# Kernel optimization log

Hardware: AMD Instinct MI355X
Metric: run time of the kernel (lower is better)

## Reference

```python
import jax, jax.numpy as jnp
import numpy as np

N_NODES = 50000
N_EDGES = 500000
N_GRAPHS = 16
C_IN = 2
CO_T = 64
CO_S = 16
K = 3


def conv_glu(x, w, b):
    # x: (N, Cin, T), w: (2*Cout, Cin, K), b: (2*Cout,) -> (N, Cout, T-K+1)
    y = jax.lax.conv_general_dilated(x, w, (1,), 'VALID',
                                     dimension_numbers=('NCH', 'OIH', 'NCH'))
    y = y + b[None, :, None]
    a, g = jnp.split(y, 2, axis=1)
    return a * jax.nn.sigmoid(g)


def gcn_relu(x, W, b, row, col, n_nodes):
    # GCNConv with self-loops, unit edge weights, applied to all T slices at once.
    # x: (N, Cin, T), W: (Cin, Cout), b: (Cout,)
    xw = jnp.einsum('nct,cd->ndt', x, W)  # (N, Cout, T)
    deg = jnp.zeros((n_nodes,), x.dtype).at[col].add(1.0) + 1.0  # +1 self loop
    dinv = deg ** -0.5
    coef = (dinv[row] * dinv[col])[:, None, None]
    msg = xw[row] * coef                   # (E, Cout, T) gather
    agg = jax.ops.segment_sum(msg, col, num_segments=n_nodes)
    agg = agg + xw * (dinv ** 2)[:, None, None]  # self-loop term
    return jax.nn.relu(agg + b[None, :, None])


def gap(x, batch, n_graphs):
    # global mean pool over nodes per graph; x: (N, C, T) -> (B, C, T)
    s = jax.ops.segment_sum(x, batch, num_segments=n_graphs)
    cnt = jax.ops.segment_sum(jnp.ones((x.shape[0],), x.dtype), batch, num_segments=n_graphs)
    return s / jnp.maximum(cnt, 1.0)[:, None, None]


def setup_inputs() -> dict:
    key = jax.random.key(0)
    ks = jax.random.split(key, 16)
    x = jax.random.normal(ks[0], (N_NODES, C_IN, 12), dtype=jnp.float32)
    edge_index = jax.random.randint(ks[1], (2, N_EDGES), 0, N_NODES)
    batch = jnp.sort(jax.random.randint(ks[2], (N_NODES,), 0, N_GRAPHS))

    def conv_p(k, cin, cout):
        k1, k2 = jax.random.split(k)
        fan = cin * K
        bound = 1.0 / np.sqrt(fan)
        w = jax.random.uniform(k1, (2 * cout, cin, K), jnp.float32, -bound, bound)
        b = jax.random.uniform(k2, (2 * cout,), jnp.float32, -bound, bound)
        return w, b

    w_t1a, b_t1a = conv_p(ks[3], C_IN, CO_T)
    w_t1b, b_t1b = conv_p(ks[4], CO_S, CO_T)
    w_t2a, b_t2a = conv_p(ks[5], CO_T, CO_T)
    w_t2b, b_t2b = conv_p(ks[6], CO_S, CO_T)

    def gcn_p(k, cin, cout):
        k1, k2 = jax.random.split(k)
        w = jax.random.normal(k1, (cin, cout), jnp.float32) * (1.0 / np.sqrt(cin))
        b = jnp.zeros((cout,), jnp.float32)
        return w, b

    w_s1, bb_s1 = gcn_p(ks[7], CO_T, CO_S)
    w_s2, bb_s2 = gcn_p(ks[8], CO_T, CO_S)

    return dict(x=x, edge_index=edge_index, batch=batch,
                w_t1a=w_t1a, b_t1a=b_t1a, w_s1=w_s1, bb_s1=bb_s1,
                w_t1b=w_t1b, b_t1b=b_t1b, w_t2a=w_t2a, b_t2a=b_t2a,
                w_s2=w_s2, bb_s2=bb_s2, w_t2b=w_t2b, b_t2b=b_t2b)


def reference(x, edge_index, batch, w_t1a, b_t1a, w_s1, bb_s1, w_t1b, b_t1b,
              w_t2a, b_t2a, w_s2, bb_s2, w_t2b, b_t2b):
    row, col = edge_index[0], edge_index[1]
    h = conv_glu(x, w_t1a, b_t1a)                     # (N, 64, 10)
    h = gcn_relu(h, w_s1, bb_s1, row, col, N_NODES)   # (N, 16, 10)
    h = conv_glu(h, w_t1b, b_t1b)                     # (N, 64, 8)
    h = conv_glu(h, w_t2a, b_t2a)                     # (N, 64, 6)
    h = gcn_relu(h, w_s2, bb_s2, row, col, N_NODES)   # (N, 16, 6)
    h = gap(h, batch, N_GRAPHS)                       # (B, 16, 6)
    out = conv_glu(h, w_t2b, b_t2b)                   # (B, 64, 4)
    return out
```

## Files before the change

kernel.cpp:

```cpp
#include <hip/hip_runtime.h>
#include <hip/hip_bf16.h>


#define NN 50000
#define NE 500000
#define NG 16
#define CAP 64

typedef __attribute__((ext_vector_type(8))) short bf16x8;
typedef __attribute__((ext_vector_type(8))) unsigned short u16x8;
typedef __attribute__((ext_vector_type(4))) float f32x4;

__device__ __forceinline__ float sigf(float g) {
    return 1.0f / (1.0f + __expf(-g));
}

__device__ __forceinline__ unsigned short to_bf16(float f) {
    __bf16 b = (__bf16)f;
    return __builtin_bit_cast(unsigned short, b);
}

__device__ __forceinline__ float from_bf16(unsigned short u) {
    return __uint_as_float(((unsigned)u) << 16);
}

__global__ void k_fill(const int* __restrict__ row, const int* __restrict__ col,
                       int* __restrict__ cnt, unsigned short* __restrict__ bucket,
                       int E)
{
    int e = blockIdx.x * 256 + threadIdx.x;
    if (e >= E) return;
    int c = col[e];
    int pos = atomicAdd(&cnt[c], 1);
    if (pos < CAP) bucket[(size_t)c * CAP + pos] = (unsigned short)row[e];
}

__global__ void k_prep2(const float* __restrict__ w1b, const float* __restrict__ w2a,
                        const float* __restrict__ ws2,
                        unsigned short* __restrict__ A2h,
                        unsigned short* __restrict__ A3h,
                        unsigned short* __restrict__ APh)
{
    int idx = blockIdx.x * 256 + threadIdx.x;
    if (idx < 1024) {
        int lane = idx & 63; int r = idx >> 6; int s = r & 1; int T = r >> 1;
        int m = T * 16 + (lane & 15); int g = lane >> 4;
        for (int i = 0; i < 8; ++i) {
            int k = s * 32 + 8 * g + i;
            float w = 0.f;
            if (k < 48) { int ci = k & 15, kk = k >> 4; w = w1b[m * 48 + ci * 3 + kk]; }
            A2h[idx * 8 + i] = to_bf16(w);
        }
    }
    if (idx < 3072) {
        int lane = idx & 63; int r = idx >> 6; int s = r % 6; int T = r / 6;
        int m = T * 16 + (lane & 15); int g = lane >> 4;
        for (int i = 0; i < 8; ++i) {
            int k = s * 32 + 8 * g + i;
            int ci = k & 63, kk = k >> 6;
            A3h[idx * 8 + i] = to_bf16(w2a[m * 192 + ci * 3 + kk]);
        }
    }
    if (idx < 128) {
        int lane = idx & 63; int s = idx >> 6;
        int d = lane & 15; int g = lane >> 4;
        for (int i = 0; i < 8; ++i) {
            int co = s * 32 + 8 * g + i;
            APh[idx * 8 + i] = to_bf16(ws2[co * 16 + d]);
        }
    }
}

__global__ __launch_bounds__(256) void k_conv1_proj2(
    const float* __restrict__ x, const float* __restrict__ w,
    const float* __restrict__ b, const float* __restrict__ W1,
    const int* __restrict__ cnt, unsigned short* __restrict__ xwb, int nNodes)
{
    __shared__ float pk[64 * 28];
    __shared__ float bs[128];
    int tid = threadIdx.x;
    for (int i = tid; i < 1792; i += 256) {
        int c = i / 28, q = i - c * 28;
        float v;
        if (q < 6)       v = w[c * 6 + q];
        else if (q < 12) v = w[(c + 64) * 6 + (q - 6)];
        else             v = W1[c * 16 + (q - 12)];
        pk[i] = v;
    }
    if (tid < 128) bs[tid] = b[tid];
    __syncthreads();

    int idx = blockIdx.x * 256 + tid;
    if (idx >= nNodes * 5) return;
    int n = idx / 5, p = idx - n * 5;
    int t0 = 2 * p;

    float xq[2][4];
#pragma unroll
    for (int ci = 0; ci < 2; ++ci) {
        const float* xp = &x[n * 24 + ci * 12 + t0];
        float2 u0 = *(const float2*)(xp);
        float2 u1 = *(const float2*)(xp + 2);
        xq[ci][0] = u0.x; xq[ci][1] = u0.y; xq[ci][2] = u1.x; xq[ci][3] = u1.y;
    }

    float acc0[16], acc1[16];
#pragma unroll
    for (int d = 0; d < 16; ++d) { acc0[d] = 0.f; acc1[d] = 0.f; }

    for (int c = 0; c < 64; ++c) {
        const float* P = &pk[c * 28];
        float4 A = *(const float4*)(P);
        float4 B = *(const float4*)(P + 4);
        float4 C = *(const float4*)(P + 8);
        float bc = bs[c], bg = bs[c + 64];

        float a0 = bc, g0 = bg;
        a0 = fmaf(A.x, xq[0][0], a0); a0 = fmaf(A.y, xq[0][1], a0); a0 = fmaf(A.z, xq[0][2], a0);
        a0 = fmaf(A.w, xq[1][0], a0); a0 = fmaf(B.x, xq[1][1], a0); a0 = fmaf(B.y, xq[1][2], a0);
        g0 = fmaf(B.z, xq[0][0], g0); g0 = fmaf(B.w, xq[0][1], g0); g0 = fmaf(C.x, xq[0][2], g0);
        g0 = fmaf(C.y, xq[1][0], g0); g0 = fmaf(C.z, xq[1][1], g0); g0 = fmaf(C.w, xq[1][2], g0);
        float h0 = a0 * sigf(g0);

        float a1 = bc, g1 = bg;
        a1 = fmaf(A.x, xq[0][1], a1); a1 = fmaf(A.y, xq[0][2], a1); a1 = fmaf(A.z, xq[0][3], a1);
        a1 = fmaf(A.w, xq[1][1], a1); a1 = fmaf(B.x, xq[1][2], a1); a1 = fmaf(B.y, xq[1][3], a1);
        g1 = fmaf(B.z, xq[0][1], g1); g1 = fmaf(B.w, xq[0][2], g1); g1 = fmaf(C.x, xq[0][3], g1);
        g1 = fmaf(C.y, xq[1][1], g1); g1 = fmaf(C.z, xq[1][2], g1); g1 = fmaf(C.w, xq[1][3], g1);
        float h1 = a1 * sigf(g1);

        float4 D = *(const float4*)(P + 12);
        float4 E = *(const float4*)(P + 16);
        float4 F = *(const float4*)(P + 20);
        float4 G = *(const float4*)(P + 24);
        float wr[16] = {D.x, D.y, D.z, D.w, E.x, E.y, E.z, E.w,
                        F.x, F.y, F.z, F.w, G.x, G.y, G.z, G.w};
#pragma unroll
        for (int d = 0; d < 16; ++d) {
            acc0[d] = fmaf(wr[d], h0, acc0[d]);
            acc1[d] = fmaf(wr[d], h1, acc1[d]);
        }
    }
    float dv = rsqrtf((float)cnt[n] + 1.0f);
    u16x8 p0, p1, p2_, p3_;
#pragma unroll
    for (int d = 0; d < 8; ++d) {
        p0[d]  = to_bf16(acc0[d] * dv);
        p1[d]  = to_bf16(acc0[d + 8] * dv);
        p2_[d] = to_bf16(acc1[d] * dv);
        p3_[d] = to_bf16(acc1[d + 8] * dv);
    }
    unsigned short* o = &xwb[n * 160 + t0 * 16];
    *(u16x8*)(o)      = p0;
    *(u16x8*)(o + 8)  = p1;
    *(u16x8*)(o + 16) = p2_;
    *(u16x8*)(o + 24) = p3_;
}

template <int W8>
__global__ __launch_bounds__(256) void k_gather_bf(
    const unsigned short* __restrict__ xs, const unsigned short* __restrict__ bucket,
    const int* __restrict__ cnt, const float* __restrict__ bias,
    unsigned short* __restrict__ hb, int total)
{
    constexpr int W = W8 * 8;
    int idx = blockIdx.x * 256 + threadIdx.x;
    if (idx >= total) return;
    int c = idx / W8, ch = idx - c * W8;
    const int deg = min(cnt[c], CAP);
    const size_t choff = (size_t)ch * 8;

    float acc[8];
#pragma unroll
    for (int i = 0; i < 8; ++i) acc[i] = 0.f;

    for (int j = 0; j < deg; j += 4) {
        ushort4 id4 = *(const ushort4*)&bucket[(size_t)c * CAP + j];
        {
            u16x8 v = *(const u16x8*)&xs[(size_t)id4.x * W + choff];
#pragma unroll
            for (int i = 0; i < 8; ++i) acc[i] += from_bf16(v[i]);
        }
        if (j + 1 < deg) {
            u16x8 v = *(const u16x8*)&xs[(size_t)id4.y * W + choff];
#pragma unroll
            for (int i = 0; i < 8; ++i) acc[i] += from_bf16(v[i]);
        }
        if (j + 2 < deg) {
            u16x8 v = *(const u16x8*)&xs[(size_t)id4.z * W + choff];
#pragma unroll
            for (int i = 0; i < 8; ++i) acc[i] += from_bf16(v[i]);
        }
        if (j + 3 < deg) {
            u16x8 v = *(const u16x8*)&xs[(size_t)id4.w * W + choff];
#pragma unroll
            for (int i = 0; i < 8; ++i) acc[i] += from_bf16(v[i]);
        }
    }

    const float dv = rsqrtf((float)cnt[c] + 1.0f);
    u16x8 sv = *(const u16x8*)&xs[(size_t)c * W + choff];
    const float* bp = &bias[(ch & 1) * 8];
    float4 b0 = *(const float4*)(bp);
    float4 b1 = *(const float4*)(bp + 4);
    float bb[8] = {b0.x, b0.y, b0.z, b0.w, b1.x, b1.y, b1.z, b1.w};
    u16x8 o;
#pragma unroll
    for (int i = 0; i < 8; ++i)
        o[i] = to_bf16(fmaxf(dv * (acc[i] + from_bf16(sv[i])) + bb[i], 0.f));
    *(u16x8*)&hb[(size_t)c * W + choff] = o;
}

__global__ __launch_bounds__(256) void k_conv23_v18(
    const unsigned short* __restrict__ h2b,
    const unsigned short* __restrict__ A2h, const float* __restrict__ b1b,
    const unsigned short* __restrict__ A3h, const float* __restrict__ b2a,
    const unsigned short* __restrict__ APh, const int* __restrict__ cnt,
    unsigned short* __restrict__ xw2b)
{
    __shared__ unsigned short H[11520];

    const int tid  = threadIdx.x;
    const int wid  = tid >> 6;
    const int lane = tid & 63;
    const int base = blockIdx.x * 16;

    unsigned short* H2 = H;
    unsigned short* H3 = H;

    const int nn   = lane & 15;
    const int nb   = nn >> 3;
    const int tt   = nn & 7;
    const int g    = lane >> 4;
    const int rowb = g * 4;

    for (int i = tid; i < 320; i += 256) {
        int ns = i / 20, rem = i - ns * 20;
        int t = rem >> 1, ci0 = (rem & 1) * 8;
        u16x8 v = *(const u16x8*)&h2b[(size_t)(base + ns) * 160 + t * 16 + ci0];
        *(u16x8*)&H2[ns * 288 + t * 24 + ci0] = v;
    }
    if (tid < 64) {
        int ns = tid >> 2, rem = tid & 3;
        int rrow = 10 + (rem >> 1), ci0 = (rem & 1) * 8;
        u16x8 z8 = (u16x8){0,0,0,0,0,0,0,0};
        *(u16x8*)&H2[ns * 288 + rrow * 24 + ci0] = z8;
    }
    __syncthreads();

    f32x4 a2[8][2];
    {
        float4 b0 = *(const float4*)&b1b[wid * 16 + rowb];
        float4 b1 = *(const float4*)&b1b[(wid + 4) * 16 + rowb];
#pragma unroll
        for (int b = 0; b < 8; ++b) {
            a2[b][0] = (f32x4){b0.x, b0.y, b0.z, b0.w};
            a2[b][1] = (f32x4){b1.x, b1.y, b1.z, b1.w};
        }
    }

#pragma unroll
    for (int s = 0; s < 2; ++s) {
        const int cib = 8 * (g & 1);
        const int kk  = 2 * s + (g >> 1);
        bf16x8 ah0 = *(const bf16x8*)&A2h[((wid * 2 + s) * 64 + lane) * 8];
        bf16x8 ah1 = *(const bf16x8*)&A2h[(((wid + 4) * 2 + s) * 64 + lane) * 8];
#pragma unroll
        for (int b = 0; b < 8; ++b) {
            const int o = (2 * b + nb) * 288 + (tt + kk) * 24 + cib;
            bf16x8 bh = *(const bf16x8*)&H2[o];
            a2[b][0] = __builtin_amdgcn_mfma_f32_16x16x32_bf16(ah0, bh, a2[b][0], 0, 0, 0);
            a2[b][1] = __builtin_amdgcn_mfma_f32_16x16x32_bf16(ah1, bh, a2[b][1], 0, 0, 0);
        }
    }
    __syncthreads();

    {
#pragma unroll
        for (int b = 0; b < 8; ++b) {
            const int wb = (2 * b + nb) * 720 + tt * 72 + wid * 16 + rowb;
            float v0 = a2[b][0][0] * sigf(a2[b][1][0]);
            float v1 = a2[b][0][1] * sigf(a2[b][1][1]);
            float v2 = a2[b][0][2] * sigf(a2[b][1][2]);
            float v3 = a2[b][0][3] * sigf(a2[b][1][3]);
            *(ushort4*)&H3[wb] = make_ushort4(to_bf16(v0), to_bf16(v1),
                                              to_bf16(v2), to_bf16(v3));
        }
        for (int z = tid; z < 512; z += 256) {
            int ns = z / 32, rem = z % 32;
            int rrow = 8 + rem / 16, c4 = (rem % 16) * 4;
            *(ushort4*)&H3[ns * 720 + rrow * 72 + c4] = make_ushort4(0, 0, 0, 0);
        }
    }
    __syncthreads();

    f32x4 a3[8][2];
    {
        float4 b0 = *(const float4*)&b2a[wid * 16 + rowb];
        float4 b1 = *(const float4*)&b2a[(wid + 4) * 16 + rowb];
#pragma unroll
        for (int b = 0; b < 8; ++b) {
            a3[b][0] = (f32x4){b0.x, b0.y, b0.z, b0.w};
            a3[b][1] = (f32x4){b1.x, b1.y, b1.z, b1.w};
        }
    }

#pragma unroll
    for (int s = 0; s < 6; ++s) {
        const int kbase = s * 32 + 8 * g;
        const int cib = kbase & 63;
        const int kk  = kbase >> 6;
        bf16x8 ah0 = *(const bf16x8*)&A3h[((wid * 6 + s) * 64 + lane) * 8];
        bf16x8 ah1 = *(const bf16x8*)&A3h[(((wid + 4) * 6 + s) * 64 + lane) * 8];
#pragma unroll
        for (int b = 0; b < 8; ++b) {
            const int o = (2 * b + nb) * 720 + (tt + kk) * 72 + cib;
            bf16x8 bh = *(const bf16x8*)&H3[o];
            a3[b][0] = __builtin_amdgcn_mfma_f32_16x16x32_bf16(ah0, bh, a3[b][0], 0, 0, 0);
            a3[b][1] = __builtin_amdgcn_mfma_f32_16x16x32_bf16(ah1, bh, a3[b][1], 0, 0, 0);
        }
    }
    __syncthreads();

    {
#pragma unroll
        for (int b = 0; b < 8; ++b) {
            const int wb = (2 * b + nb) * 720 + tt * 72 + wid * 16 + rowb;
            float v0 = a3[b][0][0] * sigf(a3[b][1][0]);
            float v1 = a3[b][0][1] * sigf(a3[b][1][1]);
            float v2 = a3[b][0][2] * sigf(a3[b][1][2]);
            float v3 = a3[b][0][3] * sigf(a3[b][1][3]);
            *(ushort4*)&H3[wb] = make_ushort4(to_bf16(v0), to_bf16(v1),
                                              to_bf16(v2), to_bf16(v3));
        }
    }
    __syncthreads();

    f32x4 ap0 = (f32x4){0.f, 0.f, 0.f, 0.f};
    f32x4 ap1 = (f32x4){0.f, 0.f, 0.f, 0.f};
#pragma unroll
    for (int s = 0; s < 2; ++s) {
        const int cob = s * 32 + 8 * g;
        bf16x8 ah = *(const bf16x8*)&APh[(s * 64 + lane) * 8];
        {
            const int b = 2 * wid;
            const int o = (2 * b + nb) * 720 + tt * 72 + cob;
            bf16x8 bh = *(const bf16x8*)&H3[o];
            ap0 = __builtin_amdgcn_mfma_f32_16x16x32_bf16(ah, bh, ap0, 0, 0, 0);
        }
        {
            const int b = 2 * wid + 1;
            const int o = (2 * b + nb) * 720 + tt * 72 + cob;
            bf16x8 bh = *(const bf16x8*)&H3[o];
            ap1 = __builtin_amdgcn_mfma_f32_16x16x32_bf16(ah, bh, ap1, 0, 0, 0);
        }
    }

    if (tt < 6) {
        {
            const int ng = base + 2 * (2 * wid) + nb;
            const float dv = rsqrtf((float)cnt[ng] + 1.0f);
            ushort4 o = make_ushort4(to_bf16(ap0[0] * dv), to_bf16(ap0[1] * dv),
                                     to_bf16(ap0[2] * dv), to_bf16(ap0[3] * dv));
            *(ushort4*)&xw2b[(size_t)ng * 96 + tt * 16 + rowb] = o;
        }
        {
            const int ng = base + 2 * (2 * wid + 1) + nb;
            const float dv = rsqrtf((float)cnt[ng] + 1.0f);
            ushort4 o = make_ushort4(to_bf16(ap1[0] * dv), to_bf16(ap1[1] * dv),
                                     to_bf16(ap1[2] * dv), to_bf16(ap1[3] * dv));
            *(ushort4*)&xw2b[(size_t)ng * 96 + tt * 16 + rowb] = o;
        }
    }
}

__global__ __launch_bounds__(128) void k_pool(
    const unsigned short* __restrict__ h5b, const int* __restrict__ batch,
    float* __restrict__ pool, int nNodes)
{
    int j = threadIdx.x;
    if (j >= 96) return;
    int n0 = blockIdx.x * 64;
    int n1 = min(n0 + 64, nNodes);
    int cur = batch[n0];
    float acc = 0.f;
    for (int n = n0; n < n1; ++n) {
        int g = batch[n];
        if (g != cur) { atomicAdd(&pool[cur * 96 + j], acc); acc = 0.f; cur = g; }
        acc += from_bf16(h5b[(size_t)n * 96 + j]);
    }
    atomicAdd(&pool[cur * 96 + j], acc);
}

__global__ __launch_bounds__(256) void k_final(
    const float* __restrict__ pool, const int* __restrict__ batch,
    const float* __restrict__ w, const float* __restrict__ b,
    float* __restrict__ out, int nNodes)
{
    __shared__ float m[96];
    __shared__ float ws[6144];
    __shared__ float bs[128];
    int g = blockIdx.x, tid = threadIdx.x;

    int lo = 0, hi = nNodes;
    while (lo < hi) { int mid = (lo + hi) >> 1; if (batch[mid] < g) lo = mid + 1; else hi = mid; }
    int lo2 = lo, hi2 = nNodes;
    while (lo2 < hi2) { int mid = (lo2 + hi2) >> 1; if (batch[mid] < g + 1) lo2 = mid + 1; else hi2 = mid; }
    float cntg = fmaxf((float)(lo2 - lo), 1.0f);

    if (tid < 96) m[tid] = pool[g * 96 + tid] / cntg;
    for (int i = tid; i < 6144; i += 256) ws[i] = w[i];
    if (tid < 128) bs[tid] = b[tid];
    __syncthreads();

    int c = tid >> 2, t = tid & 3;
    float a = bs[c], gg = bs[c + 64];
#pragma unroll
    for (int ci = 0; ci < 16; ++ci)
#pragma unroll
        for (int k = 0; k < 3; ++k) {
            float xv = m[(t + k) * 16 + ci];
            a  = fmaf(ws[c * 48 + ci * 3 + k],        xv, a);
            gg = fmaf(ws[(c + 64) * 48 + ci * 3 + k], xv, gg);
        }
    out[g * 256 + c * 4 + t] = a * sigf(gg);
}

extern "C" void kernel_launch(void* const* d_in, const int* in_sizes, int n_in,
                              void* d_out, int out_size, void* d_ws, size_t ws_size,
                              hipStream_t stream)
{
    const float* x      = (const float*)d_in[0];
    const int*   ei     = (const int*)  d_in[1];
    const int*   batch  = (const int*)  d_in[2];
    const float* w_t1a  = (const float*)d_in[3];
    const float* b_t1a  = (const float*)d_in[4];
    const float* w_s1   = (const float*)d_in[5];
    const float* bb_s1  = (const float*)d_in[6];
    const float* w_t1b  = (const float*)d_in[7];
    const float* b_t1b  = (const float*)d_in[8];
    const float* w_t2a  = (const float*)d_in[9];
    const float* b_t2a  = (const float*)d_in[10];
    const float* w_s2   = (const float*)d_in[11];
    const float* bb_s2  = (const float*)d_in[12];
    const float* w_t2b  = (const float*)d_in[13];
    const float* b_t2b  = (const float*)d_in[14];
    float* out = (float*)d_out;

    const int* row = ei;
    const int* col = ei + NE;

    unsigned short* U   = (unsigned short*)d_ws;
    unsigned short* xwb = U;
    unsigned short* hb  = xwb + (size_t)NN * 160;
    unsigned short* A2h = hb + (size_t)NN * 160;
    unsigned short* A3h = A2h + 8192;
    unsigned short* APh = A3h + 24576;
    float* pool = (float*)(APh + 1024);
    int*   cnt  = (int*)(pool + NG * 96);
    unsigned short* bucket = (unsigned short*)(cnt + NN);

    hipMemsetAsync(pool, 0, (size_t)(NG * 96 + NN) * sizeof(float), stream);

    k_fill<<<(NE + 255) / 256, 256, 0, stream>>>(row, col, cnt, bucket, NE);
    k_prep2<<<12, 256, 0, stream>>>(w_t1b, w_t2a, w_s2, A2h, A3h, APh);

    k_conv1_proj2<<<(NN * 5 + 255) / 256, 256, 0, stream>>>(
        x, w_t1a, b_t1a, w_s1, cnt, xwb, NN);

    k_gather_bf<20><<<(NN * 20 + 255) / 256, 256, 0, stream>>>(
        xwb, bucket, cnt, bb_s1, hb, NN * 20);

    k_conv23_v18<<<NN / 16, 256, 0, stream>>>(
        hb, A2h, b_t1b, A3h, b_t2a, APh, cnt, xwb);

    k_gather_bf<12><<<(NN * 12 + 255) / 256, 256, 0, stream>>>(
        xwb, bucket, cnt, bb_s2, hb, NN * 12);

    k_pool<<<(NN + 63) / 64, 128, 0, stream>>>(hb, batch, pool, NN);
    k_final<<<NG, 256, 0, stream>>>(pool, batch, w_t2b, b_t2b, out, NN);
}
```

Baseline: 219.2 us.

## Fuse first GCN gather into conv23 kernel prologue

The first GCN neighbor-gather/aggregation kernel is folded into the load stage of the conv23 kernel, so aggregated features go straight into shared memory instead of round-tripping through a global buffer. This drops one kernel launch and one write plus read of the N×160 bf16 intermediate. Buffer roles are swapped so xw2 now lands in hb and the second gather writes into xwb. The cost is that only 320 of the 256-thread block's work items do the irregular gather, with 64 threads doing a second pass, so latency-bound gathers now sit inside a heavier, lower-occupancy kernel.

```diff
diff --git a/kernel.cpp b/kernel.cpp
--- a/kernel.cpp
+++ b/kernel.cpp
@@ -211,11 +211,12 @@
     *(u16x8*)&hb[(size_t)c * W + choff] = o;
 }
 
-__global__ __launch_bounds__(256) void k_conv23_v18(
-    const unsigned short* __restrict__ h2b,
+__global__ __launch_bounds__(256) void k_conv23_v19(
+    const unsigned short* __restrict__ xw1b, const unsigned short* __restrict__ bucket,
+    const int* __restrict__ cnt, const float* __restrict__ bias1,
     const unsigned short* __restrict__ A2h, const float* __restrict__ b1b,
     const unsigned short* __restrict__ A3h, const float* __restrict__ b2a,
-    const unsigned short* __restrict__ APh, const int* __restrict__ cnt,
+    const unsigned short* __restrict__ APh,
     unsigned short* __restrict__ xw2b)
 {
     __shared__ unsigned short H[11520];
@@ -236,9 +237,51 @@
 
     for (int i = tid; i < 320; i += 256) {
         int ns = i / 20, rem = i - ns * 20;
+        int c = base + ns;
+        const int deg = min(cnt[c], CAP);
+        const size_t choff = (size_t)rem * 8;
+
+        float acc[8];
+#pragma unroll
+        for (int q = 0; q < 8; ++q) acc[q] = 0.f;
+
+        for (int j = 0; j < deg; j += 4) {
+            ushort4 id4 = *(const ushort4*)&bucket[(size_t)c * CAP + j];
+            {
+                u16x8 v = *(const u16x8*)&xw1b[(size_t)id4.x * 160 + choff];
+#pragma unroll
+                for (int q = 0; q < 8; ++q) acc[q] += from_bf16(v[q]);
+            }
+            if (j + 1 < deg) {
+                u16x8 v = *(const u16x8*)&xw1b[(size_t)id4.y * 160 + choff];
+#pragma unroll
+                for (int q = 0; q < 8; ++q) acc[q] += from_bf16(v[q]);
+            }
+            if (j + 2 < deg) {
+                u16x8 v = *(const u16x8*)&xw1b[(size_t)id4.z * 160 + choff];
+#pragma unroll
+                for (int q = 0; q < 8; ++q) acc[q] += from_bf16(v[q]);
+            }
+            if (j + 3 < deg) {
+                u16x8 v = *(const u16x8*)&xw1b[(size_t)id4.w * 160 + choff];
+#pragma unroll
+                for (int q = 0; q < 8; ++q) acc[q] += from_bf16(v[q]);
+            }
+        }
+
+        const float dv = rsqrtf((float)cnt[c] + 1.0f);
+        u16x8 sv = *(const u16x8*)&xw1b[(size_t)c * 160 + choff];
+        const float* bp = &bias1[(rem & 1) * 8];
+        float4 b0 = *(const float4*)(bp);
+        float4 b1 = *(const float4*)(bp + 4);
+        float bb[8] = {b0.x, b0.y, b0.z, b0.w, b1.x, b1.y, b1.z, b1.w};
+        u16x8 o;
+#pragma unroll
+        for (int q = 0; q < 8; ++q)
+            o[q] = to_bf16(fmaxf(dv * (acc[q] + from_bf16(sv[q])) + bb[q], 0.f));
+
         int t = rem >> 1, ci0 = (rem & 1) * 8;
-        u16x8 v = *(const u16x8*)&h2b[(size_t)(base + ns) * 160 + t * 16 + ci0];
-        *(u16x8*)&H2[ns * 288 + t * 24 + ci0] = v;
+        *(u16x8*)&H2[ns * 288 + t * 24 + ci0] = o;
     }
     if (tid < 64) {
         int ns = tid >> 2, rem = tid & 3;
@@ -468,15 +511,12 @@
     k_conv1_proj2<<<(NN * 5 + 255) / 256, 256, 0, stream>>>(
         x, w_t1a, b_t1a, w_s1, cnt, xwb, NN);
 
-    k_gather_bf<20><<<(NN * 20 + 255) / 256, 256, 0, stream>>>(
-        xwb, bucket, cnt, bb_s1, hb, NN * 20);
-
-    k_conv23_v18<<<NN / 16, 256, 0, stream>>>(
-        hb, A2h, b_t1b, A3h, b_t2a, APh, cnt, xwb);
+    k_conv23_v19<<<NN / 16, 256, 0, stream>>>(
+        xwb, bucket, cnt, bb_s1, A2h, b_t1b, A3h, b_t2a, APh, hb);
 
     k_gather_bf<12><<<(NN * 12 + 255) / 256, 256, 0, stream>>>(
-        xwb, bucket, cnt, bb_s2, hb, NN * 12);
-
-    k_pool<<<(NN + 63) / 64, 128, 0, stream>>>(hb, batch, pool, NN);
+        hb, bucket, cnt, bb_s2, xwb, NN * 12);
+
+    k_pool<<<(NN + 63) / 64, 128, 0, stream>>>(xwb, batch, pool, NN);
     k_final<<<NG, 256, 0, stream>>>(pool, batch, w_t2b, b_t2b, out, NN);
 }
```

Measured after the change: 242.9 us. +10.8%, slower.
